# Kernel optimization log

Measured on AMD Instinct MI355X. Metric: run time of the kernel, lower is better.

The kernel has to match this reference:

```python
import jax, jax.numpy as jnp
import numpy as np

BLOCK = 32          # QLinearLPBQ block_size
W_BITS = 4          # low-precision blockwise weight quantization
ACT_BITS = 16       # ActivationQDQ(bits=16)


def act_qdq(x):
    # per-tensor symmetric 16-bit fake quant-dequant (dynamic absmax scale)
    qmax = 2.0 ** (ACT_BITS - 1) - 1.0  # 32767
    scale = jnp.maximum(jnp.max(jnp.abs(x)) / qmax, 1e-12)
    return jnp.clip(jnp.round(x / scale), -qmax - 1.0, qmax) * scale


def fixed_qdq_u16(x):
    # FixedActivationQDQ: scale = 1/65536, zero_point = 0, unsigned 16-bit grid
    scale = 1.0 / 65536.0
    return jnp.clip(jnp.round(x / scale), 0.0, 65535.0) * scale


def lpbq_dequant(w):
    # blockwise (per output row, per 32-wide input block) 4-bit fake quant-dequant
    O, I = w.shape
    qmax = 2.0 ** (W_BITS - 1) - 1.0  # 7
    wb = w.reshape(O, I // BLOCK, BLOCK)
    s = jnp.maximum(jnp.max(jnp.abs(wb), axis=-1, keepdims=True) / qmax, 1e-12)
    wq = jnp.clip(jnp.round(wb / s), -qmax - 1.0, qmax) * s
    return wq.reshape(O, I)


def setup_inputs() -> dict:
    key = jax.random.key(0)
    k1, k2, k3, k4 = jax.random.split(key, 4)
    B, S, H, I = 2, 4096, 1024, 3072
    x = jax.random.normal(k1, (B, S, H), jnp.float32)
    w_gate = jax.random.normal(k2, (I, H), jnp.float32) * 0.02
    w_up = jax.random.normal(k3, (I, H), jnp.float32) * 0.02
    w_down = jax.random.normal(k4, (H, I), jnp.float32) * 0.02
    return {"x": x, "w_gate": w_gate, "w_up": w_up, "w_down": w_down}


def reference(x, w_gate, w_up, w_down):
    # x: [B, S, H]
    x = act_qdq(x)                                        # up_proj_input_qdq
    up = act_qdq(x @ lpbq_dequant(w_up).T)                # up_proj + output qdq -> [B,S,I]
    gate = act_qdq(x @ lpbq_dequant(w_gate).T)            # gate_proj + output qdq
    sig = fixed_qdq_u16(jax.nn.sigmoid(gate))             # sigmoid on fixed u16 grid
    gate = act_qdq(gate * sig)                            # SiLU (x*sigmoid) + qdq
    o = act_qdq(gate * up)                                # down_proj_input_qdq
    return o @ lpbq_dequant(w_down).T                     # [B, S, H]
```

## Files before the change

kernel.cpp:

```cpp
#include <hip/hip_runtime.h>
#include <hip/hip_bf16.h>
#include <stdint.h>


#define M_ROWS 8192
#define H_DIM 1024
#define I_DIM 3072

typedef unsigned short u16;
typedef unsigned int u32;
typedef __attribute__((ext_vector_type(8))) short bf16x8;
typedef __attribute__((ext_vector_type(4))) float f32x4;

__device__ __forceinline__ float bf2f(u16 v) { return __uint_as_float(((u32)v) << 16); }
__device__ __forceinline__ u16 f2bf(float f) {
  u32 u = __float_as_uint(f);
  u32 r = (u + 0x7fffu + ((u >> 16) & 1u)) >> 16;
  return (u16)r;
}
__device__ __forceinline__ float qdq16i(float x, float inv, float s) {
  float q = rintf(x * inv);
  q = fminf(fmaxf(q, -32768.f), 32767.f);
  return q * s;
}
__device__ __forceinline__ float sigq(float g) {
  float sig = __builtin_amdgcn_rcpf(1.f + __expf(-g));
  return fminf(fmaxf(rintf(sig * 65536.f), 0.f), 65535.f) * (1.f / 65536.f);
}

__device__ __forceinline__ float scale_read(const u32* __restrict__ scal, int s) {
  u32 m = 0;
#pragma unroll
  for (int j = 0; j < 16; ++j) m = max(m, scal[j * 16 + s]);
  return fmaxf(__uint_as_float(m) / 32767.f, 1e-12f);
}

__device__ __forceinline__ void load_lds16(const u16* g, u16* lds) {
  __builtin_amdgcn_global_load_lds(
      (const __attribute__((address_space(1))) u32*)g,
      (__attribute__((address_space(3))) u32*)lds, 16, 0, 0);
}

__device__ __forceinline__ void block_amax_atomic(float mx, u32* scal, int s) {
#pragma unroll
  for (int off = 32; off; off >>= 1) mx = fmaxf(mx, __shfl_xor(mx, off));
  __shared__ float red[4];
  const int lane = threadIdx.x & 63, wave = threadIdx.x >> 6;
  if (lane == 0) red[wave] = mx;
  __syncthreads();
  if (threadIdx.x == 0) {
    float m = fmaxf(fmaxf(red[0], red[1]), fmaxf(red[2], red[3]));
    atomicMax(scal + (blockIdx.x & 15) * 16 + s, __float_as_uint(m));
  }
}

__device__ __forceinline__ void block_amax2(float a, float b, u32* scal, int sa, int sb) {
#pragma unroll
  for (int off = 32; off; off >>= 1) {
    a = fmaxf(a, __shfl_xor(a, off));
    b = fmaxf(b, __shfl_xor(b, off));
  }
  __shared__ float red2[2][4];
  const int lane = threadIdx.x & 63, wave = threadIdx.x >> 6;
  if (lane == 0) { red2[0][wave] = a; red2[1][wave] = b; }
  __syncthreads();
  if (threadIdx.x == 0) {
    float ma = fmaxf(fmaxf(red2[0][0], red2[0][1]), fmaxf(red2[0][2], red2[0][3]));
    float mb = fmaxf(fmaxf(red2[1][0], red2[1][1]), fmaxf(red2[1][2], red2[1][3]));
    u32* base = scal + (blockIdx.x & 15) * 16;
    atomicMax(base + sa, __float_as_uint(ma));
    atomicMax(base + sb, __float_as_uint(mb));
  }
}

template <int K>
__device__ __forceinline__ void gemm_core(const u16* __restrict__ Ablk,
                                          const u16* __restrict__ Bblk,
                                          f32x4 acc[4][4], u16* smem) {
  u16* As = smem;
  u16* Bs = smem + 4096;
  const int tid = threadIdx.x;
  const int lane = tid & 63, wave = tid >> 6;
  const int wm = wave >> 1, wn = wave & 1;
  const int quad = lane >> 4, mrow = lane & 15;

  const int c0 = tid, c1 = tid + 256;
  const int r0 = c0 >> 2, g0 = ((c0 & 3) ^ ((r0 >> 1) & 3)) * 8;
  const int r1 = c1 >> 2, g1 = ((c1 & 3) ^ ((r1 >> 1) & 3)) * 8;
  const u16* a0 = Ablk + (size_t)r0 * K + g0;
  const u16* a1 = Ablk + (size_t)r1 * K + g1;
  const u16* b0 = Bblk + (size_t)r0 * K + g0;
  const u16* b1 = Bblk + (size_t)r1 * K + g1;
  u16* lA0 = &As[c0 * 8];
  u16* lA1 = &As[c1 * 8];
  u16* lB0 = &Bs[c0 * 8];
  u16* lB1 = &Bs[c1 * 8];

  int aoff[4], boff[4];
  const int lq = (quad ^ ((mrow >> 1) & 3)) * 8;
#pragma unroll
  for (int t = 0; t < 4; ++t) {
    aoff[t] = (wm * 64 + t * 16 + mrow) * 32 + lq;
    boff[t] = (wn * 64 + t * 16 + mrow) * 32 + lq;
  }

  for (int k0 = 0; k0 < K; k0 += 32) {
    __syncthreads();
    load_lds16(a0 + k0, lA0);
    load_lds16(a1 + k0, lA1);
    load_lds16(b0 + k0, lB0);
    load_lds16(b1 + k0, lB1);
    __syncthreads();
    bf16x8 af[4], bfr[4];
#pragma unroll
    for (int t = 0; t < 4; ++t) {
      af[t] = *(const bf16x8*)&As[aoff[t]];
      bfr[t] = *(const bf16x8*)&Bs[boff[t]];
    }
#pragma unroll
    for (int i = 0; i < 4; ++i)
#pragma unroll
      for (int j = 0; j < 4; ++j)
        acc[i][j] = __builtin_amdgcn_mfma_f32_16x16x32_bf16(af[i], bfr[j], acc[i][j], 0, 0, 0);
  }
}

#define HSTRIDE 136

__global__ void __launch_bounds__(256) kgemm1(const u16* __restrict__ xq,
                                              const u16* __restrict__ wcat,
                                              u16* __restrict__ up, u16* __restrict__ gh,
                                              u32* __restrict__ scal) {
  __shared__ __align__(16) u16 smem[8192];
  __shared__ __align__(16) u16 hbuf[128 * HSTRIDE];
  const int tileN = blockIdx.x * 128;
  const int tileM = blockIdx.y * 128;
  const int lane = threadIdx.x & 63, wave = threadIdx.x >> 6;
  const int wm = wave >> 1, wn = wave & 1;
  const int rb = (lane >> 4) * 4, cb = lane & 15;
  const int erow = lane >> 2, echk = lane & 3;
  u16* wbase = smem + wave * 1152;
  const u16* rbase = wbase + erow * 72;
  const u16* Ablk = xq + (size_t)tileM * H_DIM;
  f32x4 acc[4][4];

#pragma unroll
  for (int i = 0; i < 4; ++i)
#pragma unroll
    for (int j = 0; j < 4; ++j) acc[i][j] = (f32x4){0.f, 0.f, 0.f, 0.f};
  gemm_core<H_DIM>(Ablk, wcat + (size_t)(I_DIM + tileN) * H_DIM, acc, smem);
  {
    float mxg = 0.f, mxh = 0.f;
#pragma unroll
    for (int i = 0; i < 4; ++i) {
      __syncthreads();
#pragma unroll
      for (int j = 0; j < 4; ++j)
#pragma unroll
        for (int r = 0; r < 4; ++r) {
          float g = acc[i][j][r];
          mxg = fmaxf(mxg, fabsf(g));
          wbase[(rb + r) * 72 + j * 16 + cb] = f2bf(g);
          float ha = g * sigq(g);
          mxh = fmaxf(mxh, fabsf(ha));
          hbuf[(wm * 64 + i * 16 + rb + r) * HSTRIDE + wn * 64 + j * 16 + cb] = f2bf(ha);
        }
      __syncthreads();
      uint4 v0 = *(const uint4*)(rbase + echk * 8);
      uint4 v1 = *(const uint4*)(rbase + (echk + 4) * 8);
      size_t grow = (size_t)(tileM + wm * 64 + i * 16 + erow) * I_DIM + (tileN + wn * 64);
      *(uint4*)(gh + grow + echk * 8) = v0;
      *(uint4*)(gh + grow + (echk + 4) * 8) = v1;
    }
    block_amax2(mxg, mxh, scal, 2, 3);
  }

#pragma unroll
  for (int i = 0; i < 4; ++i)
#pragma unroll
    for (int j = 0; j < 4; ++j) acc[i][j] = (f32x4){0.f, 0.f, 0.f, 0.f};
  gemm_core<H_DIM>(Ablk, wcat + (size_t)tileN * H_DIM, acc, smem);
  {
    float mxu = 0.f, mxo = 0.f;
#pragma unroll
    for (int i = 0; i < 4; ++i) {
      __syncthreads();
#pragma unroll
      for (int j = 0; j < 4; ++j)
#pragma unroll
        for (int r = 0; r < 4; ++r) {
          float u = acc[i][j][r];
          mxu = fmaxf(mxu, fabsf(u));
          wbase[(rb + r) * 72 + j * 16 + cb] = f2bf(u);
          float ha = bf2f(hbuf[(wm * 64 + i * 16 + rb + r) * HSTRIDE + wn * 64 + j * 16 + cb]);
          mxo = fmaxf(mxo, fabsf(ha * u));
        }
      __syncthreads();
      uint4 v0 = *(const uint4*)(rbase + echk * 8);
      uint4 v1 = *(const uint4*)(rbase + (echk + 4) * 8);
      size_t grow = (size_t)(tileM + wm * 64 + i * 16 + erow) * I_DIM + (tileN + wn * 64);
      *(uint4*)(up + grow + echk * 8) = v0;
      *(uint4*)(up + grow + (echk + 4) * 8) = v1;
    }
    block_amax2(mxu, mxo, scal, 1, 4);
  }
}

__global__ void __launch_bounds__(256) kgemm2(const u16* __restrict__ oq,
                                              const u16* __restrict__ wdq,
                                              float* __restrict__ out) {
  __shared__ __align__(16) u16 smem[8192];
  const int tileN = blockIdx.x * 128;
  const int tileM = blockIdx.y * 128;
  f32x4 acc[4][4];
#pragma unroll
  for (int i = 0; i < 4; ++i)
#pragma unroll
    for (int j = 0; j < 4; ++j) acc[i][j] = (f32x4){0.f, 0.f, 0.f, 0.f};
  gemm_core<I_DIM>(oq + (size_t)tileM * I_DIM, wdq + (size_t)tileN * I_DIM, acc, smem);

  const int lane = threadIdx.x & 63, wave = threadIdx.x >> 6;
  const int wm = wave >> 1, wn = wave & 1;
  const int rb = (lane >> 4) * 4, cb = lane & 15;
#pragma unroll
  for (int i = 0; i < 4; ++i) {
#pragma unroll
    for (int j = 0; j < 4; ++j) {
      size_t base = (size_t)(tileM + wm * 64 + i * 16 + rb) * H_DIM +
                    (size_t)(tileN + wn * 64 + j * 16 + cb);
#pragma unroll
      for (int r = 0; r < 4; ++r) out[base + (size_t)r * H_DIM] = acc[i][j][r];
    }
  }
}

__global__ void __launch_bounds__(256) kprep(const float* __restrict__ x,
                                             const float* __restrict__ wu,
                                             const float* __restrict__ wg,
                                             const float* __restrict__ wdn,
                                             u16* __restrict__ wcat, u16* __restrict__ wdq,
                                             u32* __restrict__ scal) {
  if (blockIdx.x < 1024) {
    const float4* x4 = (const float4*)x;
    const int n4 = (M_ROWS * H_DIM) / 4;
    float mx = 0.f;
    for (int i = blockIdx.x * 256 + threadIdx.x; i < n4; i += 1024 * 256) {
      float4 v = x4[i];
      mx = fmaxf(fmaxf(fabsf(v.x), fabsf(v.y)), fmaxf(fmaxf(fabsf(v.z), fabsf(v.w)), mx));
    }
    block_amax_atomic(mx, scal, 0);
    return;
  }
  const int gid = (blockIdx.x - 1024) * 256 + threadIdx.x;
  const int unit = gid >> 3, l8 = gid & 7;
  const float* src;
  u16* dst;
  int u;
  if (unit < 98304)       { src = wu;  dst = wcat;            u = unit; }
  else if (unit < 196608) { src = wg;  dst = wcat + 3145728;  u = unit - 98304; }
  else                    { src = wdn; dst = wdq;             u = unit - 196608; }
  const size_t off = (size_t)u * 32 + (size_t)l8 * 4;
  float4 v = *(const float4*)(src + off);
  float m = fmaxf(fmaxf(fabsf(v.x), fabsf(v.y)), fmaxf(fabsf(v.z), fabsf(v.w)));
  m = fmaxf(m, __shfl_xor(m, 1));
  m = fmaxf(m, __shfl_xor(m, 2));
  m = fmaxf(m, __shfl_xor(m, 4));
  const float s = fmaxf(m / 7.0f, 1e-12f);
  const float inv = 1.0f / s;
  float vv[4] = {v.x, v.y, v.z, v.w};
  u16 o[4];
#pragma unroll
  for (int e = 0; e < 4; ++e) {
    float q = rintf(vv[e] * inv);
    q = fminf(fmaxf(q, -8.f), 7.f);
    o[e] = f2bf(q * s);
  }
  *(ushort4*)(dst + off) = make_ushort4(o[0], o[1], o[2], o[3]);
}

__global__ void __launch_bounds__(256) kqdqx(const float4* __restrict__ x,
                                             ushort4* __restrict__ xq,
                                             const u32* __restrict__ scal) {
  const float s = scale_read(scal, 0);
  const float inv = 1.0f / s;
  const int i = blockIdx.x * 256 + threadIdx.x;
  float4 v = x[i];
  ushort4 o;
  o.x = f2bf(qdq16i(v.x, inv, s));
  o.y = f2bf(qdq16i(v.y, inv, s));
  o.z = f2bf(qdq16i(v.z, inv, s));
  o.w = f2bf(qdq16i(v.w, inv, s));
  xq[i] = o;
}

#define GH4 ((M_ROWS * I_DIM) / 8)
#define EW_BLOCKS 2048

__global__ void __launch_bounds__(256) kmulo(uint4* __restrict__ gh, const uint4* __restrict__ up,
                                             u32* __restrict__ scal) {
  const float sg = scale_read(scal, 2), ig = 1.0f / sg;
  const float sh = scale_read(scal, 3), ih = 1.0f / sh;
  const float su = scale_read(scal, 1), iu = 1.0f / su;
  const float so = scale_read(scal, 4), io = 1.0f / so;
  for (int i = blockIdx.x * 256 + threadIdx.x; i < GH4; i += EW_BLOCKS * 256) {
    union { uint4 v; u16 us[8]; } a, b;
    a.v = gh[i];
    b.v = up[i];
#pragma unroll
    for (int e = 0; e < 8; ++e) {
      float g = qdq16i(bf2f(a.us[e]), ig, sg);
      float h = g * sigq(g);
      float o = qdq16i(h, ih, sh) * qdq16i(bf2f(b.us[e]), iu, su);
      a.us[e] = f2bf(qdq16i(o, io, so));
    }
    gh[i] = a.v;
  }
}

extern "C" void kernel_launch(void* const* d_in, const int* in_sizes, int n_in,
                              void* d_out, int out_size, void* d_ws, size_t ws_size,
                              hipStream_t stream) {
  (void)in_sizes; (void)n_in; (void)out_size; (void)ws_size;
  const float* x   = (const float*)d_in[0];
  const float* wg  = (const float*)d_in[1];
  const float* wu  = (const float*)d_in[2];
  const float* wdn = (const float*)d_in[3];
  float* out = (float*)d_out;
  char* ws = (char*)d_ws;

  u32* scal = (u32*)ws;
  u16* xq   = (u16*)(ws + 1024);
  u16* wcat = xq + (size_t)M_ROWS * H_DIM;
  u16* wdq  = wcat + (size_t)2 * I_DIM * H_DIM;
  u16* up   = wdq + (size_t)H_DIM * I_DIM;
  u16* gh   = up + (size_t)M_ROWS * I_DIM;

  hipMemsetAsync(scal, 0, 1024, stream);
  kprep<<<1024 + 9216, 256, 0, stream>>>(x, wu, wg, wdn, wcat, wdq, scal);
  kqdqx<<<(M_ROWS * H_DIM) / 4 / 256, 256, 0, stream>>>((const float4*)x, (ushort4*)xq, scal);
  kgemm1<<<dim3(24, 64), 256, 0, stream>>>(xq, wcat, up, gh, scal);
  kmulo<<<EW_BLOCKS, 256, 0, stream>>>((uint4*)gh, (const uint4*)up, scal);
  kgemm2<<<dim3(8, 64), 256, 0, stream>>>(gh, wdq, out);
}
```

Baseline: 352.1 us.

## Fuse gate and up GEMMs into one K-loop and widen K tile to 64

The first GEMM kernel now computes the gate and up projections in a single K loop, sharing each loaded A tile across both weight tiles. It no longer runs two sequential GEMMs with an LDS buffer holding the SiLU intermediate between them. Both GEMM cores now step through K in 64-wide tiles with an 8-chunk XOR swizzle, which halves the number of barrier pairs per K. The trade-off is higher register pressure (two 4x4 accumulator sets) and more LDS per block, which may reduce occupancy.

Result: slower. 393.8 us (+11.9%).

```diff
diff --git a/kernel.cpp b/kernel.cpp
--- a/kernel.cpp
+++ b/kernel.cpp
@@ -54,162 +54,208 @@
   }
 }
 
-__device__ __forceinline__ void block_amax2(float a, float b, u32* scal, int sa, int sb) {
+__device__ __forceinline__ void block_amax4(float a, float b, float c, float d,
+                                            u32* __restrict__ scal) {
 #pragma unroll
   for (int off = 32; off; off >>= 1) {
     a = fmaxf(a, __shfl_xor(a, off));
     b = fmaxf(b, __shfl_xor(b, off));
-  }
-  __shared__ float red2[2][4];
+    c = fmaxf(c, __shfl_xor(c, off));
+    d = fmaxf(d, __shfl_xor(d, off));
+  }
+  __shared__ float red4[4][4];
   const int lane = threadIdx.x & 63, wave = threadIdx.x >> 6;
-  if (lane == 0) { red2[0][wave] = a; red2[1][wave] = b; }
+  if (lane == 0) {
+    red4[0][wave] = a;
+    red4[1][wave] = b;
+    red4[2][wave] = c;
+    red4[3][wave] = d;
+  }
   __syncthreads();
   if (threadIdx.x == 0) {
-    float ma = fmaxf(fmaxf(red2[0][0], red2[0][1]), fmaxf(red2[0][2], red2[0][3]));
-    float mb = fmaxf(fmaxf(red2[1][0], red2[1][1]), fmaxf(red2[1][2], red2[1][3]));
     u32* base = scal + (blockIdx.x & 15) * 16;
-    atomicMax(base + sa, __float_as_uint(ma));
-    atomicMax(base + sb, __float_as_uint(mb));
+#pragma unroll
+    for (int s = 0; s < 4; ++s) {
+      float m = fmaxf(fmaxf(red4[s][0], red4[s][1]), fmaxf(red4[s][2], red4[s][3]));
+      atomicMax(base + 1 + s, __float_as_uint(m));
+    }
   }
 }
 
 template <int K>
-__device__ __forceinline__ void gemm_core(const u16* __restrict__ Ablk,
-                                          const u16* __restrict__ Bblk,
-                                          f32x4 acc[4][4], u16* smem) {
+__device__ __forceinline__ void gemm_core64(const u16* __restrict__ Ablk,
+                                            const u16* __restrict__ Bblk,
+                                            f32x4 acc[4][4], u16* smem) {
   u16* As = smem;
-  u16* Bs = smem + 4096;
+  u16* Bs = smem + 8192;
   const int tid = threadIdx.x;
   const int lane = tid & 63, wave = tid >> 6;
   const int wm = wave >> 1, wn = wave & 1;
   const int quad = lane >> 4, mrow = lane & 15;
 
-  const int c0 = tid, c1 = tid + 256;
-  const int r0 = c0 >> 2, g0 = ((c0 & 3) ^ ((r0 >> 1) & 3)) * 8;
-  const int r1 = c1 >> 2, g1 = ((c1 & 3) ^ ((r1 >> 1) & 3)) * 8;
-  const u16* a0 = Ablk + (size_t)r0 * K + g0;
-  const u16* a1 = Ablk + (size_t)r1 * K + g1;
-  const u16* b0 = Bblk + (size_t)r0 * K + g0;
-  const u16* b1 = Bblk + (size_t)r1 * K + g1;
-  u16* lA0 = &As[c0 * 8];
-  u16* lA1 = &As[c1 * 8];
-  u16* lB0 = &Bs[c0 * 8];
-  u16* lB1 = &Bs[c1 * 8];
-
-  int aoff[4], boff[4];
-  const int lq = (quad ^ ((mrow >> 1) & 3)) * 8;
+  int goff[4], loff[4];
 #pragma unroll
   for (int t = 0; t < 4; ++t) {
-    aoff[t] = (wm * 64 + t * 16 + mrow) * 32 + lq;
-    boff[t] = (wn * 64 + t * 16 + mrow) * 32 + lq;
-  }
-
-  for (int k0 = 0; k0 < K; k0 += 32) {
-    __syncthreads();
-    load_lds16(a0 + k0, lA0);
-    load_lds16(a1 + k0, lA1);
-    load_lds16(b0 + k0, lB0);
-    load_lds16(b1 + k0, lB1);
-    __syncthreads();
-    bf16x8 af[4], bfr[4];
+    const int c = tid + 256 * t;
+    const int r = c >> 3, q = c & 7;
+    goff[t] = r * K + ((q ^ (r & 7)) << 3);
+    loff[t] = c << 3;
+  }
+  const int pc0 = (quad ^ (mrow & 7)) << 3;
+  const int pc1 = ((quad + 4) ^ (mrow & 7)) << 3;
+  int arow[4], brow[4];
+#pragma unroll
+  for (int i = 0; i < 4; ++i) {
+    arow[i] = (wm * 64 + i * 16 + mrow) << 6;
+    brow[i] = (wn * 64 + i * 16 + mrow) << 6;
+  }
+
+  for (int k0 = 0; k0 < K; k0 += 64) {
+    __syncthreads();
 #pragma unroll
     for (int t = 0; t < 4; ++t) {
-      af[t] = *(const bf16x8*)&As[aoff[t]];
-      bfr[t] = *(const bf16x8*)&Bs[boff[t]];
-    }
-#pragma unroll
-    for (int i = 0; i < 4; ++i)
-#pragma unroll
-      for (int j = 0; j < 4; ++j)
-        acc[i][j] = __builtin_amdgcn_mfma_f32_16x16x32_bf16(af[i], bfr[j], acc[i][j], 0, 0, 0);
-  }
-}
-
-#define HSTRIDE 136
+      load_lds16(Ablk + k0 + goff[t], As + loff[t]);
+      load_lds16(Bblk + k0 + goff[t], Bs + loff[t]);
+    }
+    __syncthreads();
+#pragma unroll
+    for (int kk = 0; kk < 2; ++kk) {
+      const int pc = kk ? pc1 : pc0;
+      bf16x8 af[4], bfr[4];
+#pragma unroll
+      for (int t = 0; t < 4; ++t) {
+        af[t] = *(const bf16x8*)&As[arow[t] + pc];
+        bfr[t] = *(const bf16x8*)&Bs[brow[t] + pc];
+      }
+#pragma unroll
+      for (int i = 0; i < 4; ++i)
+#pragma unroll
+        for (int j = 0; j < 4; ++j)
+          acc[i][j] = __builtin_amdgcn_mfma_f32_16x16x32_bf16(af[i], bfr[j], acc[i][j], 0, 0, 0);
+    }
+  }
+}
 
 __global__ void __launch_bounds__(256) kgemm1(const u16* __restrict__ xq,
                                               const u16* __restrict__ wcat,
                                               u16* __restrict__ up, u16* __restrict__ gh,
                                               u32* __restrict__ scal) {
-  __shared__ __align__(16) u16 smem[8192];
-  __shared__ __align__(16) u16 hbuf[128 * HSTRIDE];
+  __shared__ __align__(16) u16 smem[24576];
+  u16* As = smem;
+  u16* Bus = smem + 8192;
+  u16* Bgs = smem + 16384;
   const int tileN = blockIdx.x * 128;
   const int tileM = blockIdx.y * 128;
-  const int lane = threadIdx.x & 63, wave = threadIdx.x >> 6;
+  const int tid = threadIdx.x;
+  const int lane = tid & 63, wave = tid >> 6;
   const int wm = wave >> 1, wn = wave & 1;
+  const int quad = lane >> 4, mrow = lane & 15;
+
+  const u16* Ablk = xq + (size_t)tileM * H_DIM;
+  const u16* Bublk = wcat + (size_t)tileN * H_DIM;
+  const u16* Bgblk = wcat + (size_t)(I_DIM + tileN) * H_DIM;
+
+  int goff[4], loff[4];
+#pragma unroll
+  for (int t = 0; t < 4; ++t) {
+    const int c = tid + 256 * t;
+    const int r = c >> 3, q = c & 7;
+    goff[t] = r * H_DIM + ((q ^ (r & 7)) << 3);
+    loff[t] = c << 3;
+  }
+  const int pc0 = (quad ^ (mrow & 7)) << 3;
+  const int pc1 = ((quad + 4) ^ (mrow & 7)) << 3;
+  int arow[4], brow[4];
+#pragma unroll
+  for (int i = 0; i < 4; ++i) {
+    arow[i] = (wm * 64 + i * 16 + mrow) << 6;
+    brow[i] = (wn * 64 + i * 16 + mrow) << 6;
+  }
+
+  f32x4 accg[4][4], accu[4][4];
+#pragma unroll
+  for (int i = 0; i < 4; ++i)
+#pragma unroll
+    for (int j = 0; j < 4; ++j) {
+      accg[i][j] = (f32x4){0.f, 0.f, 0.f, 0.f};
+      accu[i][j] = (f32x4){0.f, 0.f, 0.f, 0.f};
+    }
+
+  for (int k0 = 0; k0 < H_DIM; k0 += 64) {
+    __syncthreads();
+#pragma unroll
+    for (int t = 0; t < 4; ++t) {
+      load_lds16(Ablk + k0 + goff[t], As + loff[t]);
+      load_lds16(Bublk + k0 + goff[t], Bus + loff[t]);
+      load_lds16(Bgblk + k0 + goff[t], Bgs + loff[t]);
+    }
+    __syncthreads();
+#pragma unroll
+    for (int kk = 0; kk < 2; ++kk) {
+      const int pc = kk ? pc1 : pc0;
+      bf16x8 af[4], bfu[4], bfg[4];
+#pragma unroll
+      for (int t = 0; t < 4; ++t) {
+        af[t] = *(const bf16x8*)&As[arow[t] + pc];
+        bfu[t] = *(const bf16x8*)&Bus[brow[t] + pc];
+      }
+#pragma unroll
+      for (int i = 0; i < 4; ++i)
+#pragma unroll
+        for (int j = 0; j < 4; ++j)
+          accu[i][j] = __builtin_amdgcn_mfma_f32_16x16x32_bf16(af[i], bfu[j], accu[i][j], 0, 0, 0);
+#pragma unroll
+      for (int t = 0; t < 4; ++t) bfg[t] = *(const bf16x8*)&Bgs[brow[t] + pc];
+#pragma unroll
+      for (int i = 0; i < 4; ++i)
+#pragma unroll
+        for (int j = 0; j < 4; ++j)
+          accg[i][j] = __builtin_amdgcn_mfma_f32_16x16x32_bf16(af[i], bfg[j], accg[i][j], 0, 0, 0);
+    }
+  }
+
   const int rb = (lane >> 4) * 4, cb = lane & 15;
   const int erow = lane >> 2, echk = lane & 3;
-  u16* wbase = smem + wave * 1152;
-  const u16* rbase = wbase + erow * 72;
-  const u16* Ablk = xq + (size_t)tileM * H_DIM;
-  f32x4 acc[4][4];
-
-#pragma unroll
-  for (int i = 0; i < 4; ++i)
-#pragma unroll
-    for (int j = 0; j < 4; ++j) acc[i][j] = (f32x4){0.f, 0.f, 0.f, 0.f};
-  gemm_core<H_DIM>(Ablk, wcat + (size_t)(I_DIM + tileN) * H_DIM, acc, smem);
-  {
-    float mxg = 0.f, mxh = 0.f;
-#pragma unroll
-    for (int i = 0; i < 4; ++i) {
-      __syncthreads();
-#pragma unroll
-      for (int j = 0; j < 4; ++j)
-#pragma unroll
-        for (int r = 0; r < 4; ++r) {
-          float g = acc[i][j][r];
-          mxg = fmaxf(mxg, fabsf(g));
-          wbase[(rb + r) * 72 + j * 16 + cb] = f2bf(g);
-          float ha = g * sigq(g);
-          mxh = fmaxf(mxh, fabsf(ha));
-          hbuf[(wm * 64 + i * 16 + rb + r) * HSTRIDE + wn * 64 + j * 16 + cb] = f2bf(ha);
-        }
-      __syncthreads();
-      uint4 v0 = *(const uint4*)(rbase + echk * 8);
-      uint4 v1 = *(const uint4*)(rbase + (echk + 4) * 8);
-      size_t grow = (size_t)(tileM + wm * 64 + i * 16 + erow) * I_DIM + (tileN + wn * 64);
-      *(uint4*)(gh + grow + echk * 8) = v0;
-      *(uint4*)(gh + grow + (echk + 4) * 8) = v1;
-    }
-    block_amax2(mxg, mxh, scal, 2, 3);
-  }
-
-#pragma unroll
-  for (int i = 0; i < 4; ++i)
-#pragma unroll
-    for (int j = 0; j < 4; ++j) acc[i][j] = (f32x4){0.f, 0.f, 0.f, 0.f};
-  gemm_core<H_DIM>(Ablk, wcat + (size_t)tileN * H_DIM, acc, smem);
-  {
-    float mxu = 0.f, mxo = 0.f;
-#pragma unroll
-    for (int i = 0; i < 4; ++i) {
-      __syncthreads();
-#pragma unroll
-      for (int j = 0; j < 4; ++j)
-#pragma unroll
-        for (int r = 0; r < 4; ++r) {
-          float u = acc[i][j][r];
-          mxu = fmaxf(mxu, fabsf(u));
-          wbase[(rb + r) * 72 + j * 16 + cb] = f2bf(u);
-          float ha = bf2f(hbuf[(wm * 64 + i * 16 + rb + r) * HSTRIDE + wn * 64 + j * 16 + cb]);
-          mxo = fmaxf(mxo, fabsf(ha * u));
-        }
-      __syncthreads();
-      uint4 v0 = *(const uint4*)(rbase + echk * 8);
-      uint4 v1 = *(const uint4*)(rbase + (echk + 4) * 8);
-      size_t grow = (size_t)(tileM + wm * 64 + i * 16 + erow) * I_DIM + (tileN + wn * 64);
-      *(uint4*)(up + grow + echk * 8) = v0;
-      *(uint4*)(up + grow + (echk + 4) * 8) = v1;
-    }
-    block_amax2(mxu, mxo, scal, 1, 4);
-  }
+  u16* gstage = smem + wave * 1152;
+  u16* ustage = smem + 8192 + wave * 1152;
+  const u16* grb = gstage + erow * 72;
+  const u16* urb = ustage + erow * 72;
+  float mxg = 0.f, mxu = 0.f, mxh = 0.f, mxo = 0.f;
+#pragma unroll
+  for (int i = 0; i < 4; ++i) {
+    __syncthreads();
+#pragma unroll
+    for (int j = 0; j < 4; ++j)
+#pragma unroll
+      for (int r = 0; r < 4; ++r) {
+        float g = accg[i][j][r];
+        float u = accu[i][j][r];
+        mxg = fmaxf(mxg, fabsf(g));
+        mxu = fmaxf(mxu, fabsf(u));
+        float ha = g * sigq(g);
+        mxh = fmaxf(mxh, fabsf(ha));
+        mxo = fmaxf(mxo, fabsf(ha * u));
+        gstage[(rb + r) * 72 + j * 16 + cb] = f2bf(g);
+        ustage[(rb + r) * 72 + j * 16 + cb] = f2bf(u);
+      }
+    __syncthreads();
+    uint4 g0 = *(const uint4*)(grb + echk * 8);
+    uint4 g1 = *(const uint4*)(grb + (echk + 4) * 8);
+    uint4 u0 = *(const uint4*)(urb + echk * 8);
+    uint4 u1 = *(const uint4*)(urb + (echk + 4) * 8);
+    size_t grow = (size_t)(tileM + wm * 64 + i * 16 + erow) * I_DIM + (tileN + wn * 64);
+    *(uint4*)(gh + grow + echk * 8) = g0;
+    *(uint4*)(gh + grow + (echk + 4) * 8) = g1;
+    *(uint4*)(up + grow + echk * 8) = u0;
+    *(uint4*)(up + grow + (echk + 4) * 8) = u1;
+  }
+  block_amax4(mxu, mxg, mxh, mxo, scal);
 }
 
 __global__ void __launch_bounds__(256) kgemm2(const u16* __restrict__ oq,
                                               const u16* __restrict__ wdq,
                                               float* __restrict__ out) {
-  __shared__ __align__(16) u16 smem[8192];
+  __shared__ __align__(16) u16 smem[16384];
   const int tileN = blockIdx.x * 128;
   const int tileM = blockIdx.y * 128;
   f32x4 acc[4][4];
@@ -217,7 +263,7 @@
   for (int i = 0; i < 4; ++i)
 #pragma unroll
     for (int j = 0; j < 4; ++j) acc[i][j] = (f32x4){0.f, 0.f, 0.f, 0.f};
-  gemm_core<I_DIM>(oq + (size_t)tileM * I_DIM, wdq + (size_t)tileN * I_DIM, acc, smem);
+  gemm_core64<I_DIM>(oq + (size_t)tileM * I_DIM, wdq + (size_t)tileN * I_DIM, acc, smem);
 
   const int lane = threadIdx.x & 63, wave = threadIdx.x >> 6;
   const int wm = wave >> 1, wn = wave & 1;
```
